# Kernel tuning notes

Measured on AMD Instinct MI355X. Metric: run time of the kernel, lower is better.

The kernel has to match this reference:

```python
import jax, jax.numpy as jnp
import numpy as np

T, BS, NH, DS, HD, R = 1024, 4, 16, 32, 128, 8
D_INNER = NH * HD

def setup_inputs() -> dict:
    key = jax.random.key(0)
    k1, k2, k3, k4, k5 = jax.random.split(key, 5)
    return {
        "B_proj": jax.random.normal(k1, (T, BS, NH, DS, R), jnp.float32),
        "X_proj": jax.random.normal(k2, (T, BS, NH, HD, R), jnp.float32),
        "alpha_raw": jax.random.normal(k3, (T, BS, NH), jnp.float32),
        "alpha_bias": jnp.full((NH,), 2.2, jnp.float32) + 0.01 * jax.random.normal(k4, (NH,), jnp.float32),
        "z": jax.random.normal(k5, (T, BS, D_INNER), jnp.float32),
        "H0": jnp.zeros((BS, NH, DS, HD), jnp.float32),
    }

def _elman_scan(B_proj, X_proj, alpha_raw, alpha_bias, z, H0):
    # alpha in (0, 0.5): sigmoid(-softplus(.))
    alpha_all = jax.nn.sigmoid(-jax.nn.softplus(alpha_raw + alpha_bias))  # [T,B,NH]

    def step(H, inp):
        B_t, X_t, a_t, z_t = inp
        # rank-R MIMO update: [B,NH,DS,HD]
        update = jnp.einsum('bhnr,bhpr->bhnp', B_t, X_t)
        H_new = jax.nn.silu(a_t[:, :, None, None] * H + update)
        y_t = H_new.sum(axis=2).reshape(H.shape[0], -1)  # [B, d_inner]
        out_t = y_t * jax.nn.silu(z_t + y_t)
        return H_new, out_t

    H_final, output = jax.lax.scan(step, H0, (B_proj, X_proj, alpha_all, z))
    return output, H_final

def reference(B_proj, X_proj, alpha_raw, alpha_bias, z, H0):
    return _elman_scan(B_proj, X_proj, alpha_raw, alpha_bias, z, H0)
```

## Files before the change

kernel.cpp:

```cpp
#include <hip/hip_runtime.h>


namespace {
constexpr int T  = 1024;
constexpr int BS = 4;
constexpr int NH = 16;
constexpr int DS = 32;
constexpr int HD = 128;
constexpr int R  = 8;
constexpr int DI = NH * HD;
constexpr int GROUP = 4;

constexpr unsigned BF_T  = BS * NH * DS * R;
constexpr unsigned XF_T  = BS * NH * HD * R;
constexpr unsigned A_T   = BS * NH;
constexpr unsigned OUT_T = BS * DI;

constexpr int SPAN   = 64;
constexpr int WARM   = 8;
constexpr int NSLICE = 16;

constexpr float LOG2E = 1.4426950408889634f;

typedef __attribute__((ext_vector_type(8)))  _Float16 half8;
typedef __attribute__((ext_vector_type(2)))  float    f32x2;
typedef __attribute__((ext_vector_type(16))) float    f32x16;
typedef __attribute__((ext_vector_type(4)))  unsigned u32x4;

__device__ __forceinline__ float fast_exp(float x) {
    return __builtin_amdgcn_exp2f(x * LOG2E);
}
__device__ __forceinline__ float fast_silu(float x) {
    return x * __builtin_amdgcn_rcpf(1.0f + __builtin_amdgcn_exp2f(x * -LOG2E));
}

__global__ __launch_bounds__(256)
void alpha_kernel(const float* __restrict__ ar_, const float* __restrict__ ab_,
                  float* __restrict__ alpha_) {
    int i = blockIdx.x * 256 + threadIdx.x;
    float v = ar_[i] + ab_[i & (NH - 1)];
    alpha_[i] = __builtin_amdgcn_rcpf(2.0f + fast_exp(v));
}

template<bool PRE>
__global__ __launch_bounds__(256, 2)
void elman32_kernel(const float* __restrict__ B_,
                    const float* __restrict__ X_,
                    const float* __restrict__ a_,
                    const float* __restrict__ ab_,
                    const float* __restrict__ z_,
                    const float* __restrict__ H0_,
                    float* __restrict__ out_,
                    float* __restrict__ Hf_)
{
    const int lane  = threadIdx.x & 63;
    const int W     = blockIdx.x * 4 + (threadIdx.x >> 6);
    const int slice = W >> 8;
    const int Wl    = W & 255;
    const int pc    = Wl & 3;
    const int bh    = Wl >> 2;
    const int h     = bh & (NH - 1);
    const int b     = bh >> 4;
    const int l31   = lane & 31;
    const int khalf = lane >> 5;
    const int p0    = pc * 32;

    const int t_begin   = slice * SPAN - (slice ? WARM : 0);
    const int ngroups   = (slice ? (SPAN + WARM) : SPAN) / GROUP;
    const int emit_from = slice ? (WARM / GROUP) : 0;

    const unsigned mz = khalf ? 0u : 0xFFFFFFFFu;
    const float abv = PRE ? 0.0f : ab_[h];

    f32x16 H;
    if (slice == 0) {
        #pragma unroll
        for (int i = 0; i < 16; ++i) {
            int row = (i & 3) + 8 * (i >> 2) + 4 * khalf;
            H[i] = H0_[(unsigned)bh * 4096u + (unsigned)row * 128u
                       + (unsigned)(p0 + l31)];
        }
    } else {
        #pragma unroll
        for (int i = 0; i < 16; ++i) H[i] = 0.0f;
    }

    unsigned oB = (unsigned)bh * (DS * R) + (unsigned)l31 * R
                + (unsigned)t_begin * BF_T;
    unsigned oX = (unsigned)bh * (HD * R) + (unsigned)(p0 + l31) * R
                + (unsigned)t_begin * XF_T;
    unsigned oA = (unsigned)bh + (unsigned)(t_begin + (lane & 3)) * A_T;
    unsigned oZ = (unsigned)b * DI + (unsigned)h * HD + (unsigned)(p0 + l31)
                + (unsigned)t_begin * OUT_T;
    unsigned oO = oZ;

    u32x4 afr[GROUP], bfr[GROUP];
    float zr[GROUP];
    float av0, av1;

    auto pk8 = [](const float4& v0, const float4& v1) -> u32x4 {
        u32x4 u;
        u.x = __builtin_bit_cast(unsigned, __builtin_amdgcn_cvt_pkrtz(v0.x, v0.y));
        u.y = __builtin_bit_cast(unsigned, __builtin_amdgcn_cvt_pkrtz(v0.z, v0.w));
        u.z = __builtin_bit_cast(unsigned, __builtin_amdgcn_cvt_pkrtz(v1.x, v1.y));
        u.w = __builtin_bit_cast(unsigned, __builtin_amdgcn_cvt_pkrtz(v1.z, v1.w));
        return u;
    };

    auto refill = [&](int s) {
        float4 b0 = *(const float4*)(B_ + oB + (unsigned)s * BF_T);
        float4 b1 = *(const float4*)(B_ + oB + (unsigned)s * BF_T + 4u);
        float4 x0 = *(const float4*)(X_ + oX + (unsigned)s * XF_T);
        float4 x1 = *(const float4*)(X_ + oX + (unsigned)s * XF_T + 4u);
        u32x4 a = pk8(b0, b1);
        a.x &= mz; a.y &= mz; a.z &= mz; a.w &= mz;
        afr[s] = a;
        bfr[s] = pk8(x0, x1);
        zr[s]  = z_[oZ + (unsigned)s * OUT_T];
    };

    #pragma unroll
    for (int s = 0; s < GROUP; ++s) refill(s);
    av0 = a_[oA];
    av1 = a_[oA + (unsigned)GROUP * A_T];
    oA += 2u * GROUP * A_T;
    oB += GROUP * BF_T; oX += GROUP * XF_T; oZ += GROUP * OUT_T;

    auto step = [&](int s, bool emit, float av) {
        float ar = __int_as_float(
            __builtin_amdgcn_readlane(__float_as_int(av), s));
        float alpha = PRE ? ar
                          : __builtin_amdgcn_rcpf(2.0f + fast_exp(ar + abv));
        f32x16 c = H * alpha;
        f32x16 d = __builtin_amdgcn_mfma_f32_32x32x16_f16(
            __builtin_bit_cast(half8, afr[s]),
            __builtin_bit_cast(half8, bfr[s]), c, 0, 0, 0);
        f32x16 m = d * (-LOG2E);
        f32x16 e;
        #pragma unroll
        for (int i = 0; i < 16; ++i) e[i] = __builtin_amdgcn_exp2f(m[i]);
        f32x16 den = e + 1.0f;
        #pragma unroll
        for (int i = 0; i < 8; ++i) {
            float pd = den[2*i] * den[2*i+1];
            float q  = __builtin_amdgcn_rcpf(pd);
            H[2*i]   = d[2*i]   * (den[2*i+1] * q);
            H[2*i+1] = d[2*i+1] * (den[2*i]   * q);
        }
        if (emit) {
            f32x2 s0 = f32x2{H[0], H[1]}   + f32x2{H[2], H[3]};
            f32x2 s1 = f32x2{H[4], H[5]}   + f32x2{H[6], H[7]};
            f32x2 s2 = f32x2{H[8], H[9]}   + f32x2{H[10], H[11]};
            f32x2 s3 = f32x2{H[12], H[13]} + f32x2{H[14], H[15]};
            s0 += s1; s2 += s3; s0 += s2;
            float yp = s0.x + s0.y;
            float y2 = yp + __shfl_xor(yp, 32, 64);
            float gt = y2 * fast_silu(zr[s] + y2);
            if (lane < 32) out_[oO + (unsigned)s * OUT_T] = gt;
        }
    };

    auto group_body = [&](bool emit, float av) {
        #pragma unroll
        for (int s = 0; s < GROUP; ++s) {
            step(s, emit, av);
            refill(s);
        }
        oB += GROUP * BF_T; oX += GROUP * XF_T;
        oZ += GROUP * OUT_T; oO += GROUP * OUT_T;
    };

    const int P = (ngroups - 2) / 2;
    int g = 0;
    #pragma unroll 1
    for (int gg = 0; gg < P; ++gg) {
        group_body(g >= emit_from, av0);
        av0 = a_[oA];
        ++g;
        group_body(g >= emit_from, av1);
        av1 = a_[oA + (unsigned)GROUP * A_T];
        oA += 2u * GROUP * A_T;
        ++g;
    }
    group_body(true, av0);
    #pragma unroll
    for (int s = 0; s < GROUP; ++s) step(s, true, av1);

    if (slice == NSLICE - 1) {
        #pragma unroll
        for (int i = 0; i < 16; ++i) {
            int row = (i & 3) + 8 * (i >> 2) + 4 * khalf;
            Hf_[(unsigned)bh * 4096u + (unsigned)row * 128u
                + (unsigned)(p0 + l31)] = H[i];
        }
    }
}
}

extern "C" void kernel_launch(void* const* d_in, const int* in_sizes, int n_in,
                              void* d_out, int out_size, void* d_ws, size_t ws_size,
                              hipStream_t stream) {
    const float* B_proj     = (const float*)d_in[0];
    const float* X_proj     = (const float*)d_in[1];
    const float* alpha_raw  = (const float*)d_in[2];
    const float* alpha_bias = (const float*)d_in[3];
    const float* z          = (const float*)d_in[4];
    const float* H0         = (const float*)d_in[5];

    float* out = (float*)d_out;
    float* Hf  = out + (size_t)T * BS * DI;

    const size_t alpha_bytes = (size_t)T * BS * NH * sizeof(float);
    if (ws_size >= alpha_bytes) {
        float* aw = (float*)d_ws;
        alpha_kernel<<<T * BS * NH / 256, 256, 0, stream>>>(alpha_raw, alpha_bias, aw);
        elman32_kernel<true><<<1024, 256, 0, stream>>>(
            B_proj, X_proj, aw, alpha_bias, z, H0, out, Hf);
    } else {
        elman32_kernel<false><<<1024, 256, 0, stream>>>(
            B_proj, X_proj, alpha_raw, alpha_bias, z, H0, out, Hf);
    }
}
```

Baseline: 107.2 us.

## Process two 32-column tiles per wave, sharing B fragments and halving grid

Each wave now owns two 32-wide column tiles of the head state, so it issues two independent MFMAs per timestep that share one packed B fragment and one alpha value. The grid shrinks to 512 blocks and the prefetch group depth drops from 4 to 2 to hold register pressure down. The aim is more instruction-level parallelism along the serial recurrence and fewer redundant B loads. In exchange, per-wave register use rises, occupancy falls, and the shallower prefetch may expose more memory latency.

```diff
diff --git a/kernel.cpp b/kernel.cpp
--- a/kernel.cpp
+++ b/kernel.cpp
@@ -9,7 +9,7 @@
 constexpr int HD = 128;
 constexpr int R  = 8;
 constexpr int DI = NH * HD;
-constexpr int GROUP = 4;
+constexpr int GROUP = 2;
 
 constexpr unsigned BF_T  = BS * NH * DS * R;
 constexpr unsigned XF_T  = BS * NH * HD * R;
@@ -55,15 +55,16 @@
 {
     const int lane  = threadIdx.x & 63;
     const int W     = blockIdx.x * 4 + (threadIdx.x >> 6);
-    const int slice = W >> 8;
-    const int Wl    = W & 255;
-    const int pc    = Wl & 3;
-    const int bh    = Wl >> 2;
+    const int slice = W >> 7;
+    const int Wl    = W & 127;
+    const int pp    = Wl & 1;
+    const int bh    = Wl >> 1;
     const int h     = bh & (NH - 1);
     const int b     = bh >> 4;
     const int l31   = lane & 31;
     const int khalf = lane >> 5;
-    const int p0    = pc * 32;
+    const int p0a   = pp * 64;
+    const int p0b   = p0a + 32;
 
     const int t_begin   = slice * SPAN - (slice ? WARM : 0);
     const int ngroups   = (slice ? (SPAN + WARM) : SPAN) / GROUP;
@@ -72,30 +73,33 @@
     const unsigned mz = khalf ? 0u : 0xFFFFFFFFu;
     const float abv = PRE ? 0.0f : ab_[h];
 
-    f32x16 H;
+    f32x16 Ha, Hb;
     if (slice == 0) {
         #pragma unroll
         for (int i = 0; i < 16; ++i) {
             int row = (i & 3) + 8 * (i >> 2) + 4 * khalf;
-            H[i] = H0_[(unsigned)bh * 4096u + (unsigned)row * 128u
-                       + (unsigned)(p0 + l31)];
+            unsigned base = (unsigned)bh * 4096u + (unsigned)row * 128u;
+            Ha[i] = H0_[base + (unsigned)(p0a + l31)];
+            Hb[i] = H0_[base + (unsigned)(p0b + l31)];
         }
     } else {
         #pragma unroll
-        for (int i = 0; i < 16; ++i) H[i] = 0.0f;
-    }
-
-    unsigned oB = (unsigned)bh * (DS * R) + (unsigned)l31 * R
-                + (unsigned)t_begin * BF_T;
-    unsigned oX = (unsigned)bh * (HD * R) + (unsigned)(p0 + l31) * R
-                + (unsigned)t_begin * XF_T;
-    unsigned oA = (unsigned)bh + (unsigned)(t_begin + (lane & 3)) * A_T;
-    unsigned oZ = (unsigned)b * DI + (unsigned)h * HD + (unsigned)(p0 + l31)
-                + (unsigned)t_begin * OUT_T;
-    unsigned oO = oZ;
-
-    u32x4 afr[GROUP], bfr[GROUP];
-    float zr[GROUP];
+        for (int i = 0; i < 16; ++i) { Ha[i] = 0.0f; Hb[i] = 0.0f; }
+    }
+
+    unsigned oB  = (unsigned)bh * (DS * R) + (unsigned)l31 * R
+                 + (unsigned)t_begin * BF_T;
+    unsigned oXa = (unsigned)bh * (HD * R) + (unsigned)(p0a + l31) * R
+                 + (unsigned)t_begin * XF_T;
+    unsigned oXb = oXa + 32u * R;
+    unsigned oA  = (unsigned)bh + (unsigned)(t_begin + (lane & 1)) * A_T;
+    unsigned oZa = (unsigned)b * DI + (unsigned)h * HD + (unsigned)(p0a + l31)
+                 + (unsigned)t_begin * OUT_T;
+    unsigned oZb = oZa + 32u;
+    unsigned oOa = oZa, oOb = oZb;
+
+    u32x4 afr[GROUP], bfa[GROUP], bfb[GROUP];
+    float zra[GROUP], zrb[GROUP];
     float av0, av1;
 
     auto pk8 = [](const float4& v0, const float4& v1) -> u32x4 {
@@ -108,15 +112,19 @@
     };
 
     auto refill = [&](int s) {
-        float4 b0 = *(const float4*)(B_ + oB + (unsigned)s * BF_T);
-        float4 b1 = *(const float4*)(B_ + oB + (unsigned)s * BF_T + 4u);
-        float4 x0 = *(const float4*)(X_ + oX + (unsigned)s * XF_T);
-        float4 x1 = *(const float4*)(X_ + oX + (unsigned)s * XF_T + 4u);
+        float4 b0  = *(const float4*)(B_ + oB  + (unsigned)s * BF_T);
+        float4 b1  = *(const float4*)(B_ + oB  + (unsigned)s * BF_T + 4u);
+        float4 xa0 = *(const float4*)(X_ + oXa + (unsigned)s * XF_T);
+        float4 xa1 = *(const float4*)(X_ + oXa + (unsigned)s * XF_T + 4u);
+        float4 xb0 = *(const float4*)(X_ + oXb + (unsigned)s * XF_T);
+        float4 xb1 = *(const float4*)(X_ + oXb + (unsigned)s * XF_T + 4u);
         u32x4 a = pk8(b0, b1);
         a.x &= mz; a.y &= mz; a.z &= mz; a.w &= mz;
         afr[s] = a;
-        bfr[s] = pk8(x0, x1);
-        zr[s]  = z_[oZ + (unsigned)s * OUT_T];
+        bfa[s] = pk8(xa0, xa1);
+        bfb[s] = pk8(xb0, xb1);
+        zra[s] = z_[oZa + (unsigned)s * OUT_T];
+        zrb[s] = z_[oZb + (unsigned)s * OUT_T];
     };
 
     #pragma unroll
@@ -124,39 +132,58 @@
     av0 = a_[oA];
     av1 = a_[oA + (unsigned)GROUP * A_T];
     oA += 2u * GROUP * A_T;
-    oB += GROUP * BF_T; oX += GROUP * XF_T; oZ += GROUP * OUT_T;
+    oB += GROUP * BF_T; oXa += GROUP * XF_T; oXb += GROUP * XF_T;
+    oZa += GROUP * OUT_T; oZb += GROUP * OUT_T;
+
+    auto silu16 = [](const f32x16& d, f32x16& Hdst) {
+        f32x16 m = d * (-LOG2E);
+        f32x16 e;
+        #pragma unroll
+        for (int i = 0; i < 16; ++i) e[i] = __builtin_amdgcn_exp2f(m[i]);
+        f32x16 den = e + 1.0f;
+        #pragma unroll
+        for (int i = 0; i < 8; ++i) {
+            float pd = den[2*i] * den[2*i+1];
+            float q  = __builtin_amdgcn_rcpf(pd);
+            Hdst[2*i]   = d[2*i]   * (den[2*i+1] * q);
+            Hdst[2*i+1] = d[2*i+1] * (den[2*i]   * q);
+        }
+    };
+    auto tree16 = [](const f32x16& H) -> float {
+        f32x2 s0 = f32x2{H[0], H[1]}   + f32x2{H[2], H[3]};
+        f32x2 s1 = f32x2{H[4], H[5]}   + f32x2{H[6], H[7]};
+        f32x2 s2 = f32x2{H[8], H[9]}   + f32x2{H[10], H[11]};
+        f32x2 s3 = f32x2{H[12], H[13]} + f32x2{H[14], H[15]};
+        s0 += s1; s2 += s3; s0 += s2;
+        return s0.x + s0.y;
+    };
 
     auto step = [&](int s, bool emit, float av) {
         float ar = __int_as_float(
             __builtin_amdgcn_readlane(__float_as_int(av), s));
         float alpha = PRE ? ar
                           : __builtin_amdgcn_rcpf(2.0f + fast_exp(ar + abv));
-        f32x16 c = H * alpha;
-        f32x16 d = __builtin_amdgcn_mfma_f32_32x32x16_f16(
+        f32x16 ca = Ha * alpha;
+        f32x16 da = __builtin_amdgcn_mfma_f32_32x32x16_f16(
             __builtin_bit_cast(half8, afr[s]),
-            __builtin_bit_cast(half8, bfr[s]), c, 0, 0, 0);
-        f32x16 m = d * (-LOG2E);
-        f32x16 e;
-        #pragma unroll
-        for (int i = 0; i < 16; ++i) e[i] = __builtin_amdgcn_exp2f(m[i]);
-        f32x16 den = e + 1.0f;
-        #pragma unroll
-        for (int i = 0; i < 8; ++i) {
-            float pd = den[2*i] * den[2*i+1];
-            float q  = __builtin_amdgcn_rcpf(pd);
-            H[2*i]   = d[2*i]   * (den[2*i+1] * q);
-            H[2*i+1] = d[2*i+1] * (den[2*i]   * q);
-        }
+            __builtin_bit_cast(half8, bfa[s]), ca, 0, 0, 0);
+        f32x16 cb = Hb * alpha;
+        f32x16 db = __builtin_amdgcn_mfma_f32_32x32x16_f16(
+            __builtin_bit_cast(half8, afr[s]),
+            __builtin_bit_cast(half8, bfb[s]), cb, 0, 0, 0);
+        silu16(da, Ha);
+        silu16(db, Hb);
         if (emit) {
-            f32x2 s0 = f32x2{H[0], H[1]}   + f32x2{H[2], H[3]};
-            f32x2 s1 = f32x2{H[4], H[5]}   + f32x2{H[6], H[7]};
-            f32x2 s2 = f32x2{H[8], H[9]}   + f32x2{H[10], H[11]};
-            f32x2 s3 = f32x2{H[12], H[13]} + f32x2{H[14], H[15]};
-            s0 += s1; s2 += s3; s0 += s2;
-            float yp = s0.x + s0.y;
-            float y2 = yp + __shfl_xor(yp, 32, 64);
-            float gt = y2 * fast_silu(zr[s] + y2);
-            if (lane < 32) out_[oO + (unsigned)s * OUT_T] = gt;
+            float ypa = tree16(Ha);
+            float ypb = tree16(Hb);
+            float y2a = ypa + __shfl_xor(ypa, 32, 64);
+            float y2b = ypb + __shfl_xor(ypb, 32, 64);
+            float ga  = y2a * fast_silu(zra[s] + y2a);
+            float gb  = y2b * fast_silu(zrb[s] + y2b);
+            if (lane < 32) {
+                out_[oOa + (unsigned)s * OUT_T] = ga;
+                out_[oOb + (unsigned)s * OUT_T] = gb;
+            }
         }
     };
 
@@ -166,8 +193,9 @@
             step(s, emit, av);
             refill(s);
         }
-        oB += GROUP * BF_T; oX += GROUP * XF_T;
-        oZ += GROUP * OUT_T; oO += GROUP * OUT_T;
+        oB += GROUP * BF_T; oXa += GROUP * XF_T; oXb += GROUP * XF_T;
+        oZa += GROUP * OUT_T; oZb += GROUP * OUT_T;
+        oOa += GROUP * OUT_T; oOb += GROUP * OUT_T;
     };
 
     const int P = (ngroups - 2) / 2;
@@ -190,8 +218,9 @@
         #pragma unroll
         for (int i = 0; i < 16; ++i) {
             int row = (i & 3) + 8 * (i >> 2) + 4 * khalf;
-            Hf_[(unsigned)bh * 4096u + (unsigned)row * 128u
-                + (unsigned)(p0 + l31)] = H[i];
+            unsigned base = (unsigned)bh * 4096u + (unsigned)row * 128u;
+            Hf_[base + (unsigned)(p0a + l31)] = Ha[i];
+            Hf_[base + (unsigned)(p0b + l31)] = Hb[i];
         }
     }
 }
@@ -214,10 +243,10 @@
     if (ws_size >= alpha_bytes) {
         float* aw = (float*)d_ws;
         alpha_kernel<<<T * BS * NH / 256, 256, 0, stream>>>(alpha_raw, alpha_bias, aw);
-        elman32_kernel<true><<<1024, 256, 0, stream>>>(
+        elman32_kernel<true><<<512, 256, 0, stream>>>(
             B_proj, X_proj, aw, alpha_bias, z, H0, out, Hf);
     } else {
-        elman32_kernel<false><<<1024, 256, 0, stream>>>(
+        elman32_kernel<false><<<512, 256, 0, stream>>>(
             B_proj, X_proj, alpha_raw, alpha_bias, z, H0, out, Hf);
     }
 }
```

Result: no change. 107.2 us (+0.0%).

## Halve time slices, shrink group, and prefetch raw inputs two groups ahead

Applied to the files above, without the earlier changes.

Time is now split into 8 slices of 128 steps instead of 16 of 64, so the grid is 512 blocks and there is less redundant warm-up recompute. The group size drops to 2 steps. A two-stage register pipeline loads raw fp32 B/X/z one group ahead of packing, so load latency is hidden behind more compute. In exchange there is half the parallelism, a longer serial chain per wave, and more registers used for the prefetch buffers.

```diff
diff --git a/kernel.cpp b/kernel.cpp
--- a/kernel.cpp
+++ b/kernel.cpp
@@ -9,16 +9,16 @@
 constexpr int HD = 128;
 constexpr int R  = 8;
 constexpr int DI = NH * HD;
-constexpr int GROUP = 4;
+constexpr int GROUP = 2;
 
 constexpr unsigned BF_T  = BS * NH * DS * R;
 constexpr unsigned XF_T  = BS * NH * HD * R;
 constexpr unsigned A_T   = BS * NH;
 constexpr unsigned OUT_T = BS * DI;
 
-constexpr int SPAN   = 64;
+constexpr int SPAN   = 128;
 constexpr int WARM   = 8;
-constexpr int NSLICE = 16;
+constexpr int NSLICE = 8;
 
 constexpr float LOG2E = 1.4426950408889634f;
 
@@ -89,13 +89,15 @@
                 + (unsigned)t_begin * BF_T;
     unsigned oX = (unsigned)bh * (HD * R) + (unsigned)(p0 + l31) * R
                 + (unsigned)t_begin * XF_T;
-    unsigned oA = (unsigned)bh + (unsigned)(t_begin + (lane & 3)) * A_T;
+    unsigned oA = (unsigned)bh + (unsigned)(t_begin + (lane & 1)) * A_T;
     unsigned oZ = (unsigned)b * DI + (unsigned)h * HD + (unsigned)(p0 + l31)
                 + (unsigned)t_begin * OUT_T;
     unsigned oO = oZ;
 
-    u32x4 afr[GROUP], bfr[GROUP];
-    float zr[GROUP];
+    u32x4 afrP[GROUP], bfrP[GROUP];
+    float zP[GROUP];
+    float4 rB0[GROUP], rB1[GROUP], rX0[GROUP], rX1[GROUP];
+    float  zR[GROUP];
     float av0, av1;
 
     auto pk8 = [](const float4& v0, const float4& v1) -> u32x4 {
@@ -107,24 +109,32 @@
         return u;
     };
 
-    auto refill = [&](int s) {
-        float4 b0 = *(const float4*)(B_ + oB + (unsigned)s * BF_T);
-        float4 b1 = *(const float4*)(B_ + oB + (unsigned)s * BF_T + 4u);
-        float4 x0 = *(const float4*)(X_ + oX + (unsigned)s * XF_T);
-        float4 x1 = *(const float4*)(X_ + oX + (unsigned)s * XF_T + 4u);
-        u32x4 a = pk8(b0, b1);
+    auto loadR = [&](int s) {
+        rB0[s] = *(const float4*)(B_ + oB + (unsigned)s * BF_T);
+        rB1[s] = *(const float4*)(B_ + oB + (unsigned)s * BF_T + 4u);
+        rX0[s] = *(const float4*)(X_ + oX + (unsigned)s * XF_T);
+        rX1[s] = *(const float4*)(X_ + oX + (unsigned)s * XF_T + 4u);
+        zR[s]  = z_[oZ + (unsigned)s * OUT_T];
+    };
+    auto packP = [&](int s) {
+        u32x4 a = pk8(rB0[s], rB1[s]);
         a.x &= mz; a.y &= mz; a.z &= mz; a.w &= mz;
-        afr[s] = a;
-        bfr[s] = pk8(x0, x1);
-        zr[s]  = z_[oZ + (unsigned)s * OUT_T];
-    };
-
-    #pragma unroll
-    for (int s = 0; s < GROUP; ++s) refill(s);
+        afrP[s] = a;
+        bfrP[s] = pk8(rX0[s], rX1[s]);
+        zP[s]   = zR[s];
+    };
+    auto advance = [&]() {
+        oB += GROUP * BF_T; oX += GROUP * XF_T; oZ += GROUP * OUT_T;
+    };
+
+    loadR(0); loadR(1);
     av0 = a_[oA];
     av1 = a_[oA + (unsigned)GROUP * A_T];
     oA += 2u * GROUP * A_T;
-    oB += GROUP * BF_T; oX += GROUP * XF_T; oZ += GROUP * OUT_T;
+    packP(0); packP(1);
+    advance();
+    loadR(0); loadR(1);
+    advance();
 
     auto step = [&](int s, bool emit, float av) {
         float ar = __int_as_float(
@@ -133,8 +143,8 @@
                           : __builtin_amdgcn_rcpf(2.0f + fast_exp(ar + abv));
         f32x16 c = H * alpha;
         f32x16 d = __builtin_amdgcn_mfma_f32_32x32x16_f16(
-            __builtin_bit_cast(half8, afr[s]),
-            __builtin_bit_cast(half8, bfr[s]), c, 0, 0, 0);
+            __builtin_bit_cast(half8, afrP[s]),
+            __builtin_bit_cast(half8, bfrP[s]), c, 0, 0, 0);
         f32x16 m = d * (-LOG2E);
         f32x16 e;
         #pragma unroll
@@ -155,7 +165,7 @@
             s0 += s1; s2 += s3; s0 += s2;
             float yp = s0.x + s0.y;
             float y2 = yp + __shfl_xor(yp, 32, 64);
-            float gt = y2 * fast_silu(zr[s] + y2);
+            float gt = y2 * fast_silu(zP[s] + y2);
             if (lane < 32) out_[oO + (unsigned)s * OUT_T] = gt;
         }
     };
@@ -164,16 +174,17 @@
         #pragma unroll
         for (int s = 0; s < GROUP; ++s) {
             step(s, emit, av);
-            refill(s);
-        }
-        oB += GROUP * BF_T; oX += GROUP * XF_T;
-        oZ += GROUP * OUT_T; oO += GROUP * OUT_T;
-    };
-
-    const int P = (ngroups - 2) / 2;
+            packP(s);
+            loadR(s);
+        }
+        advance();
+        oO += GROUP * OUT_T;
+    };
+
+    const int P2 = (ngroups - 2) / 2;
     int g = 0;
     #pragma unroll 1
-    for (int gg = 0; gg < P; ++gg) {
+    for (int gg = 0; gg < P2; ++gg) {
         group_body(g >= emit_from, av0);
         av0 = a_[oA];
         ++g;
@@ -182,7 +193,12 @@
         oA += 2u * GROUP * A_T;
         ++g;
     }
-    group_body(true, av0);
+    #pragma unroll
+    for (int s = 0; s < GROUP; ++s) {
+        step(s, true, av0);
+        packP(s);
+    }
+    oO += GROUP * OUT_T;
     #pragma unroll
     for (int s = 0; s < GROUP; ++s) step(s, true, av1);
 
@@ -214,10 +230,10 @@
     if (ws_size >= alpha_bytes) {
         float* aw = (float*)d_ws;
         alpha_kernel<<<T * BS * NH / 256, 256, 0, stream>>>(alpha_raw, alpha_bias, aw);
-        elman32_kernel<true><<<1024, 256, 0, stream>>>(
+        elman32_kernel<true><<<512, 256, 0, stream>>>(
             B_proj, X_proj, aw, alpha_bias, z, H0, out, Hf);
     } else {
-        elman32_kernel<false><<<1024, 256, 0, stream>>>(
+        elman32_kernel<false><<<512, 256, 0, stream>>>(
             B_proj, X_proj, alpha_raw, alpha_bias, z, H0, out, Hf);
     }
 }
```

Result: no change. 107.0 us (-0.2%).
